# Optimization experiments

Measured on AMD Instinct MI355X. Metric: run time of the kernel, lower is better.

The kernel has to match this reference:

```python
import jax, jax.numpy as jnp
import numpy as np

EPS = 1e-5
SLOPE = 0.01  # LeakyReLU default
C = 512
C2 = C // 2
B, D, W, H = 2, 16, 16, 16


def _leaky(x):
    return jnp.where(x >= 0, x, SLOPE * x)


def _bn_c(x, g, b, rm, rv):
    # per-channel BN (eval mode) over axis 1 of a (B,C,...) tensor
    shape = (1, -1) + (1,) * (x.ndim - 2)
    inv = jax.lax.rsqrt(rv + EPS)
    return (x - rm.reshape(shape)) * (inv * g).reshape(shape) + b.reshape(shape)


def _bn_s(x, g, b, rm, rv):
    # scalar-feature BatchNorm1d(1) in eval mode
    return (x - rm[0]) * (jax.lax.rsqrt(rv[0] + EPS) * g[0]) + b[0]


def setup_inputs() -> dict:
    key = jax.random.key(0)
    ks = jax.random.split(key, 8)
    s = 0.02
    inp = {
        'x': jax.random.normal(ks[0], (B, C, D, W, H), jnp.float32),
        'topo_prompt': jax.random.normal(ks[1], (D, W, H, 6), jnp.float32) * s,
        # edge_aggregation_func: Linear(6,1)+BN1d(1)
        'w_ea': jax.random.normal(ks[2], (1, 6), jnp.float32) * s,
        'b_ea': jnp.zeros((1,), jnp.float32),
        'g_ea': jnp.ones((1,), jnp.float32), 'be_ea': jnp.zeros((1,), jnp.float32),
        'rm_ea': jnp.zeros((1,), jnp.float32), 'rv_ea': jnp.ones((1,), jnp.float32),
        # vertex_update_func: Linear(2C, C/2)+BN1d(C/2)
        'w_v': jax.random.normal(ks[3], (C2, 2 * C), jnp.float32) * s,
        'b_v': jnp.zeros((C2,), jnp.float32),
        'g_v': jnp.ones((C2,), jnp.float32), 'be_v': jnp.zeros((C2,), jnp.float32),
        'rm_v': jnp.zeros((C2,), jnp.float32), 'rv_v': jnp.ones((C2,), jnp.float32),
        # edge_update_func: Linear(2C, C/2)+BN1d(C/2)
        'w_e': jax.random.normal(ks[4], (C2, 2 * C), jnp.float32) * s,
        'b_e': jnp.zeros((C2,), jnp.float32),
        'g_e': jnp.ones((C2,), jnp.float32), 'be_e': jnp.zeros((C2,), jnp.float32),
        'rm_e': jnp.zeros((C2,), jnp.float32), 'rv_e': jnp.ones((C2,), jnp.float32),
        # update_edge_reduce_func: Linear(6,1)+BN1d(1)
        'w_r': jax.random.normal(ks[5], (1, 6), jnp.float32) * s,
        'b_r': jnp.zeros((1,), jnp.float32),
        'g_r': jnp.ones((1,), jnp.float32), 'be_r': jnp.zeros((1,), jnp.float32),
        'rm_r': jnp.zeros((1,), jnp.float32), 'rv_r': jnp.ones((1,), jnp.float32),
        # final_aggregation_layer: Conv3d(3C/2 -> C, k=1, bias=False)+BN3d(C)
        'w_f': jax.random.normal(ks[6], (C, C + C2), jnp.float32) * s,
        'g_f': jnp.ones((C,), jnp.float32), 'be_f': jnp.zeros((C,), jnp.float32),
        'rm_f': jnp.zeros((C,), jnp.float32), 'rv_f': jnp.ones((C,), jnp.float32),
    }
    return inp


def reference(x, topo_prompt,
              w_ea, b_ea, g_ea, be_ea, rm_ea, rv_ea,
              w_v, b_v, g_v, be_v, rm_v, rv_v,
              w_e, b_e, g_e, be_e, rm_e, rv_e,
              w_r, b_r, g_r, be_r, rm_r, rv_r,
              w_f, g_f, be_f, rm_f, rv_f):
    # 6-neighbor circular shifts: cat((x[-1:], x[:-1])) == roll(+1); cat((x[1:], x[:1])) == roll(-1)
    shifts = jnp.stack([
        jnp.roll(x, 1, axis=2), jnp.roll(x, -1, axis=2),
        jnp.roll(x, 1, axis=3), jnp.roll(x, -1, axis=3),
        jnp.roll(x, 1, axis=4), jnp.roll(x, -1, axis=4),
    ], axis=-1)  # (B,C,D,W,H,6)
    edge = shifts * x[..., None] + topo_prompt  # topo_prompt (D,W,H,6) broadcasts

    # edge aggregation: Linear(6->1) + BN1d(1) + LeakyReLU
    agg = jnp.einsum('bcdwhk,k->bcdwh', edge, w_ea[0]) + b_ea[0]
    agg = _leaky(_bn_s(agg, g_ea, be_ea, rm_ea, rv_ea))  # (B,C,D,W,H)

    # vertex update: Linear(2C->C/2) + BN + LeakyReLU
    feat_v = jnp.concatenate([x, agg], axis=1)  # (B,2C,D,W,H)
    uv = jnp.einsum('bcdwh,oc->bodwh', feat_v, w_v) + b_v[None, :, None, None, None]
    uv = _leaky(_bn_c(uv, g_v, be_v, rm_v, rv_v))  # (B,C/2,D,W,H)

    # edge update: cat(vertex x6, edge) on channel dim -> Linear(2C->C/2) + BN + LeakyReLU
    vrep = jnp.broadcast_to(x[..., None], x.shape + (6,))
    feat_e = jnp.concatenate([vrep, edge], axis=1)  # (B,2C,D,W,H,6)
    ue = jnp.einsum('bcdwhk,oc->bodwhk', feat_e, w_e) + b_e[None, :, None, None, None, None]
    ue = _leaky(_bn_c(ue, g_e, be_e, rm_e, rv_e))  # (B,C/2,D,W,H,6)

    # reduce 6 neighbors: Linear(6->1) + BN1d(1) + LeakyReLU
    ur = jnp.einsum('bodwhk,k->bodwh', ue, w_r[0]) + b_r[0]
    ur = _leaky(_bn_s(ur, g_r, be_r, rm_r, rv_r))  # (B,C/2,D,W,H)

    update_feature = uv * ur

    # final 1x1x1 conv (bias=False) + BN3d + LeakyReLU
    fused = jnp.concatenate([x, update_feature], axis=1)  # (B,3C/2,D,W,H)
    out = jnp.einsum('bcdwh,oc->bodwh', fused, w_f)
    out = _leaky(_bn_c(out, g_f, be_f, rm_f, rv_f))
    return out
```

## Files before the change

kernel.cpp:

```cpp
#include <hip/hip_runtime.h>

#define BATCH 2
#define C 512
#define C2 256
#define V 4096
#define NROWS 8192
#define EPS 1e-5f
#define SLOPE 0.01f

typedef __bf16 bf16;
typedef __bf16 bf16x8 __attribute__((ext_vector_type(8)));
typedef __bf16 bf16x4 __attribute__((ext_vector_type(4)));
typedef float  f32x4  __attribute__((ext_vector_type(4)));

__device__ __forceinline__ float leaky(float x) { return x >= 0.f ? x : SLOPE * x; }

__device__ __forceinline__ int nbr(int v, int k) {
    int h = v & 15, w = (v >> 4) & 15, d = v >> 8;
    switch (k) {
        case 0: return (v & 0x0FF) | (((d + 15) & 15) << 8);
        case 1: return (v & 0x0FF) | (((d + 1) & 15) << 8);
        case 2: return (v & 0xF0F) | (((w + 15) & 15) << 4);
        case 3: return (v & 0xF0F) | (((w + 1) & 15) << 4);
        case 4: return (v & 0xFF0) | ((h + 15) & 15);
        default: return (v & 0xFF0) | ((h + 1) & 15);
    }
}

__device__ __forceinline__ void gload16(const bf16* g, bf16* l) {
    __builtin_amdgcn_global_load_lds(
        (const __attribute__((address_space(1))) void*)g,
        (__attribute__((address_space(3))) void*)l, 16, 0, 0);
}

__device__ __forceinline__ void stage_gl64(bf16* buf, const bf16* srcbase, size_t ld,
                                           int kcol, int wv, int lane) {
    const int sslot = ((lane & 7) ^ (lane >> 3)) * 8;
    #pragma unroll
    for (int j = 0; j < 4; j++) {
        const int rl = wv * 32 + j * 8;
        gload16(srcbase + (size_t)(rl + (lane >> 3)) * ld + kcol + sslot,
                buf + rl * 64);
    }
}

__device__ __forceinline__ void mmstep64(const bf16* A, const bf16* B,
                                         f32x4 (&acc)[4][4], int abase, int bbase,
                                         int lr, int kg)
{
    #pragma unroll
    for (int sub = 0; sub < 2; sub++) {
        const int slot = ((sub * 4 + kg) ^ (lr & 7)) * 8;
        bf16x8 af[4], bv[4];
        #pragma unroll
        for (int mb = 0; mb < 4; mb++)
            af[mb] = *(const bf16x8*)(A + (abase + mb * 16 + lr) * 64 + slot);
        #pragma unroll
        for (int nb = 0; nb < 4; nb++)
            bv[nb] = *(const bf16x8*)(B + (bbase + nb * 16 + lr) * 64 + slot);
        #pragma unroll
        for (int mb = 0; mb < 4; mb++)
            #pragma unroll
            for (int nb = 0; nb < 4; nb++)
                acc[mb][nb] = __builtin_amdgcn_mfma_f32_16x16x32_bf16(af[mb], bv[nb], acc[mb][nb], 0, 0, 0);
    }
}

__global__ __launch_bounds__(256) void k_prep(
    const float* wv, const float* we, const float* wf,
    const float* w_ea, const float* b_ea, const float* g_ea, const float* be_ea,
    const float* rm_ea, const float* rv_ea,
    const float* b_v, const float* g_v, const float* be_v, const float* rm_v, const float* rv_v,
    const float* b_e, const float* g_e, const float* be_e, const float* rm_e, const float* rv_e,
    const float* w_r, const float* b_r, const float* g_r, const float* be_r,
    const float* rm_r, const float* rv_r,
    const float* g_f, const float* be_f, const float* rm_f, const float* rv_f,
    float* P, float* obv, float* obe, float* obf,
    bf16* wmain, bf16* we2, bf16* owf)
{
    int i = blockIdx.x * 256 + threadIdx.x;
    if (i < 524288) {
        int o = i >> 10, c = i & 1023;
        float val;
        if (o < 256) val = rsqrtf(rv_v[o] + EPS) * g_v[o] * wv[(size_t)o * 1024 + c];
        else {
            int oe = o - 256;
            val = (c < 512) ? rsqrtf(rv_e[oe] + EPS) * g_e[oe] * we[(size_t)oe * 1024 + c] : 0.f;
        }
        wmain[i] = (bf16)val;
    } else if (i < 655360) {
        int j = i - 524288; int o = j >> 9, c = j & 511;
        we2[j] = (bf16)(rsqrtf(rv_e[o] + EPS) * g_e[o] * we[(size_t)o * 1024 + 512 + c]);
    } else if (i < 1048576) {
        int j = i - 655360; int o = j / 768;
        owf[j] = (bf16)(rsqrtf(rv_f[o] + EPS) * g_f[o] * wf[j]);
    }
    if (blockIdx.x == 0) {
        int t = threadIdx.x;
        obf[t]       = be_f[t]       - rsqrtf(rv_f[t]       + EPS) * g_f[t]       * rm_f[t];
        obf[t + 256] = be_f[t + 256] - rsqrtf(rv_f[t + 256] + EPS) * g_f[t + 256] * rm_f[t + 256];
        float sv = rsqrtf(rv_v[t] + EPS) * g_v[t];
        obv[t] = sv * (b_v[t] - rm_v[t]) + be_v[t];
        float se = rsqrtf(rv_e[t] + EPS) * g_e[t];
        obe[t] = se * (b_e[t] - rm_e[t]) + be_e[t];
        if (t < 6) {
            float sa = rsqrtf(rv_ea[0] + EPS) * g_ea[0];
            P[t] = sa * w_ea[t];
            float sr = rsqrtf(rv_r[0] + EPS) * g_r[0];
            P[8 + t] = sr * w_r[t];
        }
        if (t == 6) {
            float sa = rsqrtf(rv_ea[0] + EPS) * g_ea[0];
            P[6] = sa * (b_ea[0] - rm_ea[0]) + be_ea[0];
            float sr = rsqrtf(rv_r[0] + EPS) * g_r[0];
            P[14] = sr * (b_r[0] - rm_r[0]) + be_r[0];
        }
    }
}

__global__ __launch_bounds__(256) void k_aggT(
    const float* __restrict__ x, const float* __restrict__ topo,
    const float* __restrict__ P,
    bf16* __restrict__ xT, bf16* __restrict__ aggT)
{
    __shared__ float T[64][65];
    const int t = threadIdx.x;
    const int b = blockIdx.z, ct = blockIdx.y * 64, vt = blockIdx.x * 64;
    const int cl = t >> 2;
    const int c  = ct + cl;
    const int vl0 = (t & 3) * 16;
    const int v0 = vt + vl0;
    const int w = (v0 >> 4) & 15, d = v0 >> 8;
    const float* xp = x + (((size_t)b * C + c) << 12);

    float xr[16], xd0[16], xd1[16], xw0[16], xw1[16];
    #pragma unroll
    for (int i = 0; i < 4; i++) {
        float4 a;
        a = ((const float4*)(xp + v0))[i];                        xr [4*i]=a.x; xr [4*i+1]=a.y; xr [4*i+2]=a.z; xr [4*i+3]=a.w;
        a = ((const float4*)(xp + (((d+15)&15)<<8) + (w<<4)))[i]; xd0[4*i]=a.x; xd0[4*i+1]=a.y; xd0[4*i+2]=a.z; xd0[4*i+3]=a.w;
        a = ((const float4*)(xp + (((d+ 1)&15)<<8) + (w<<4)))[i]; xd1[4*i]=a.x; xd1[4*i+1]=a.y; xd1[4*i+2]=a.z; xd1[4*i+3]=a.w;
        a = ((const float4*)(xp + (d<<8) + (((w+15)&15)<<4)))[i]; xw0[4*i]=a.x; xw0[4*i+1]=a.y; xw0[4*i+2]=a.z; xw0[4*i+3]=a.w;
        a = ((const float4*)(xp + (d<<8) + (((w+ 1)&15)<<4)))[i]; xw1[4*i]=a.x; xw1[4*i+1]=a.y; xw1[4*i+2]=a.z; xw1[4*i+3]=a.w;
    }

    #pragma unroll
    for (int p = 0; p < 2; ++p) {
        float val[16];
        if (p == 0) {
            #pragma unroll
            for (int j = 0; j < 16; j++) val[j] = xr[j];
        } else {
            #pragma unroll
            for (int j = 0; j < 16; j++) {
                const float* tp = topo + (size_t)(v0 + j) * 6;
                float s = P[6];
                s = fmaf(P[0], fmaf(xd0[j], xr[j], tp[0]), s);
                s = fmaf(P[1], fmaf(xd1[j], xr[j], tp[1]), s);
                s = fmaf(P[2], fmaf(xw0[j], xr[j], tp[2]), s);
                s = fmaf(P[3], fmaf(xw1[j], xr[j], tp[3]), s);
                s = fmaf(P[4], fmaf(xr[(j+15)&15], xr[j], tp[4]), s);
                s = fmaf(P[5], fmaf(xr[(j+ 1)&15], xr[j], tp[5]), s);
                val[j] = leaky(s);
            }
        }
        __syncthreads();
        #pragma unroll
        for (int j = 0; j < 16; j++) T[cl][vl0 + j] = val[j];
        __syncthreads();
        const int vr = t >> 2, c0 = (t & 3) * 16;
        bf16x8 lo, hi;
        #pragma unroll
        for (int i = 0; i < 8; i++) {
            lo[i] = (bf16)T[c0 + i][vr];
            hi[i] = (bf16)T[c0 + 8 + i][vr];
        }
        bf16* dst = (p == 0) ? xT : aggT;
        bf16* dp = dst + ((size_t)(b << 12) + vt + vr) * C + ct + c0;
        *(bf16x8*)dp = lo;
        *(bf16x8*)(dp + 8) = hi;
    }
}

template<bool MAIN>
__device__ __forceinline__ void gemm_body(
    int m0, int n0, int kk, int nsteps,
    const bf16* __restrict__ wA, size_t ldA,
    const bf16* __restrict__ xT, const bf16* __restrict__ aggT,
    const float* __restrict__ topo, const float* __restrict__ bvp,
    bf16* __restrict__ uvT, float* __restrict__ sxe, bf16* __restrict__ se,
    bf16 (*A)[128 * 64], bf16 (*B)[128 * 64])
{
    const int t = threadIdx.x, lane = t & 63;
    const int wv = t >> 6, wmi = wv >> 1, wni = wv & 1;
    const int lr = lane & 15, kg = lane >> 4;

    const bf16* wAb  = wA + (size_t)m0 * ldA;
    const bf16* xTb  = xT + (size_t)n0 * C;
    const bf16* agTb = aggT + (size_t)n0 * C;

    const int erow = t >> 1, ecol = (t & 1) * 32;
    const bf16* pBx = nullptr; const bf16* pB2 = nullptr; float tp = 0.f;
    int eslot[4];
    if (!MAIN) {
        const int rB = n0 + erow;
        const int vvv = rB & 4095, bb = rB >> 12;
        pBx = xT + (size_t)rB * C + ecol;
        pB2 = xT + (size_t)((bb << 12) | nbr(vvv, kk)) * C + ecol;
        tp = topo[vvv * 6 + kk];
        #pragma unroll
        for (int j = 0; j < 4; j++)
            eslot[j] = ((((t & 1) * 4 + j) ^ (erow & 7)) * 8);
    }

    f32x4 acc[4][4];
    #pragma unroll
    for (int mb = 0; mb < 4; mb++)
        #pragma unroll
        for (int nb = 0; nb < 4; nb++) acc[mb][nb] = 0.f;

    uint4 bx[4], bn[4];
    auto issueB = [&](int s) {
        #pragma unroll
        for (int j = 0; j < 4; j++) {
            bx[j] = *(const uint4*)(pBx + s * 64 + j * 8);
            bn[j] = *(const uint4*)(pB2 + s * 64 + j * 8);
        }
    };
    auto commitB = [&](int buf) {
        #pragma unroll
        for (int j = 0; j < 4; j++) {
            bf16x8 xa = *(bf16x8*)&bx[j], xn = *(bf16x8*)&bn[j];
            bf16x8 e;
            #pragma unroll
            for (int i = 0; i < 8; i++)
                e[i] = (bf16)fmaf((float)xa[i], (float)xn[i], tp);
            *(bf16x8*)(&B[buf][erow * 64 + eslot[j]]) = e;
        }
    };
    auto stageStep = [&](int buf, int s) {
        stage_gl64(A[buf], wAb, ldA, s * 64, wv, lane);
        if (MAIN) {
            const bf16* src = (s < 8) ? xTb : agTb;
            stage_gl64(B[buf], src, C, (s & 7) * 64, wv, lane);
        }
    };

    stageStep(0, 0);
    if (!MAIN) { issueB(0); commitB(0); if (nsteps > 1) issueB(1); }

    int cb = 0;
    #pragma unroll 1
    for (int s = 0; s < nsteps; ++s) {
        __syncthreads();
        if (s + 1 < nsteps) stageStep(cb ^ 1, s + 1);
        mmstep64(A[cb], B[cb], acc, wmi * 64, wni * 64, lr, kg);
        if (!MAIN && s + 1 < nsteps) {
            commitB(cb ^ 1);
            if (s + 2 < nsteps) issueB(s + 2);
        }
        cb ^= 1;
    }

    if (MAIN) {
        if (m0 < 256) {
            #pragma unroll
            for (int mb = 0; mb < 4; mb++) {
                const int o = m0 + wmi * 64 + mb * 16 + kg * 4;
                f32x4 bv4 = *(const f32x4*)(bvp + o);
                #pragma unroll
                for (int nb = 0; nb < 4; nb++) {
                    const int col = n0 + wni * 64 + nb * 16 + lr;
                    bf16x4 o4;
                    #pragma unroll
                    for (int q = 0; q < 4; q++)
                        o4[q] = (bf16)leaky(acc[mb][nb][q] + bv4[q]);
                    *(bf16x4*)(uvT + (size_t)col * C2 + o) = o4;
                }
            }
        } else {
            #pragma unroll
            for (int mb = 0; mb < 4; mb++) {
                const int o = (m0 - 256) + wmi * 64 + mb * 16 + kg * 4;
                #pragma unroll
                for (int nb = 0; nb < 4; nb++) {
                    const int col = n0 + wni * 64 + nb * 16 + lr;
                    *(f32x4*)(sxe + (size_t)col * C2 + o) = acc[mb][nb];
                }
            }
        }
    } else {
        #pragma unroll
        for (int mb = 0; mb < 4; mb++) {
            const int o = m0 + wmi * 64 + mb * 16 + kg * 4;
            #pragma unroll
            for (int nb = 0; nb < 4; nb++) {
                const int col = n0 + wni * 64 + nb * 16 + lr;
                bf16x4 o4;
                #pragma unroll
                for (int q = 0; q < 4; q++) o4[q] = (bf16)acc[mb][nb][q];
                *(bf16x4*)(se + ((size_t)kk * NROWS + col) * C2 + o) = o4;
            }
        }
    }
}

__global__ __launch_bounds__(256, 2) void k_gemm(
    const bf16* __restrict__ xT, const bf16* __restrict__ aggT,
    const bf16* __restrict__ wm, const bf16* __restrict__ we2,
    const float* __restrict__ bvp, const float* __restrict__ topo,
    bf16* __restrict__ uvT, float* __restrict__ sxe, bf16* __restrict__ se)
{
    __shared__ __align__(16) bf16 A[2][128 * 64];
    __shared__ __align__(16) bf16 B[2][128 * 64];
    const int lb = (blockIdx.x & 7) * 128 + (blockIdx.x >> 3);
    const int n0 = (lb >> 4) * 128;
    const int sub = lb & 15;
    if (sub < 4) {
        const int m0 = sub * 128;
        const int nsteps = (m0 < 256) ? 16 : 8;
        gemm_body<true>(m0, n0, 0, nsteps, wm, 1024, xT, aggT, topo, bvp,
                        uvT, sxe, nullptr, A, B);
    } else {
        const int e = sub - 4;
        const int kk = e >> 1, m0 = (e & 1) * 128;
        gemm_body<false>(m0, n0, kk, 8, we2, 512, xT, aggT, topo, bvp,
                         nullptr, nullptr, se, A, B);
    }
}

__global__ __launch_bounds__(256) void k_comb(
    const float* __restrict__ sxe, const bf16* __restrict__ se,
    const bf16* __restrict__ uvT, const float* __restrict__ bep,
    const float* __restrict__ P, bf16* __restrict__ updT)
{
    const int g = blockIdx.x * 256 + threadIdx.x;
    const int row = g >> 5, o0 = (g & 31) * 8;
    const size_t base = (size_t)row * C2 + o0;

    f32x4 sx0 = *(const f32x4*)(sxe + base);
    f32x4 sx1 = *(const f32x4*)(sxe + base + 4);
    f32x4 be0 = *(const f32x4*)(bep + o0);
    f32x4 be1 = *(const f32x4*)(bep + o0 + 4);
    float ur[8] = {};
    #pragma unroll
    for (int k = 0; k < 6; k++) {
        bf16x8 s8 = *(const bf16x8*)(se + (size_t)k * NROWS * C2 + base);
        const float wrk = P[8 + k];
        #pragma unroll
        for (int i = 0; i < 4; i++) {
            ur[i]     = fmaf(wrk, leaky(sx0[i] + (float)s8[i]     + be0[i]), ur[i]);
            ur[i + 4] = fmaf(wrk, leaky(sx1[i] + (float)s8[i + 4] + be1[i]), ur[i + 4]);
        }
    }
    const float brp = P[14];
    bf16x8 uv8 = *(const bf16x8*)(uvT + base);
    bf16x8 o8;
    #pragma unroll
    for (int i = 0; i < 8; i++)
        o8[i] = (bf16)((float)uv8[i] * leaky(ur[i] + brp));
    *(bf16x8*)(updT + base) = o8;
}

__global__ __launch_bounds__(256, 2) void k_out(
    const bf16* __restrict__ xT, const bf16* __restrict__ updT,
    const bf16* __restrict__ wf, const float* __restrict__ bfp,
    float* __restrict__ out)
{
    __shared__ __align__(16) bf16 A[2][128 * 64];
    __shared__ __align__(16) bf16 B[2][128 * 64];
    const int t = threadIdx.x, lane = t & 63;
    const int wv = t >> 6, wmi = wv >> 1, wni = wv & 1;
    const int lr = lane & 15, kg = lane >> 4;
    const int lb = (blockIdx.x & 7) * 32 + (blockIdx.x >> 3);
    const int n0 = (lb >> 2) * 128, m0 = (lb & 3) * 128;

    const bf16* wAb = wf   + (size_t)m0 * 768;
    const bf16* xTb = xT   + (size_t)n0 * C;
    const bf16* uTb = updT + (size_t)n0 * C2;

    f32x4 acc[4][4];
    #pragma unroll
    for (int mb = 0; mb < 4; mb++)
        #pragma unroll
        for (int nb = 0; nb < 4; nb++) acc[mb][nb] = 0.f;

    auto stageStep = [&](int buf, int s) {
        stage_gl64(A[buf], wAb, 768, s * 64, wv, lane);
        if (s < 8) stage_gl64(B[buf], xTb, C, s * 64, wv, lane);
        else       stage_gl64(B[buf], uTb, C2, (s - 8) * 64, wv, lane);
    };

    stageStep(0, 0);
    int cb = 0;
    #pragma unroll 1
    for (int s = 0; s < 12; ++s) {
        __syncthreads();
        if (s + 1 < 12) stageStep(cb ^ 1, s + 1);
        mmstep64(A[cb], B[cb], acc, wmi * 64, wni * 64, lr, kg);
        cb ^= 1;
    }

    #pragma unroll
    for (int mb = 0; mb < 4; mb++) {
        const int o = m0 + wmi * 64 + mb * 16 + kg * 4;
        f32x4 bf4 = *(const f32x4*)(bfp + o);
        #pragma unroll
        for (int nb = 0; nb < 4; nb++) {
            const int col = n0 + wni * 64 + nb * 16 + lr;
            const int b = col >> 12, v = col & 4095;
            #pragma unroll
            for (int q = 0; q < 4; q++)
                out[(((size_t)b * C + o + q) << 12) + v] = leaky(acc[mb][nb][q] + bf4[q]);
        }
    }
}

extern "C" void kernel_launch(void* const* d_in, const int* in_sizes, int n_in,
                              void* d_out, int out_size, void* d_ws, size_t ws_size,
                              hipStream_t stream)
{
    const float* x    = (const float*)d_in[0];
    const float* topo = (const float*)d_in[1];
    const float* w_ea = (const float*)d_in[2];
    const float* b_ea = (const float*)d_in[3];
    const float* g_ea = (const float*)d_in[4];
    const float* be_ea= (const float*)d_in[5];
    const float* rm_ea= (const float*)d_in[6];
    const float* rv_ea= (const float*)d_in[7];
    const float* w_v  = (const float*)d_in[8];
    const float* b_v  = (const float*)d_in[9];
    const float* g_v  = (const float*)d_in[10];
    const float* be_v = (const float*)d_in[11];
    const float* rm_v = (const float*)d_in[12];
    const float* rv_v = (const float*)d_in[13];
    const float* w_e  = (const float*)d_in[14];
    const float* b_e  = (const float*)d_in[15];
    const float* g_e  = (const float*)d_in[16];
    const float* be_e = (const float*)d_in[17];
    const float* rm_e = (const float*)d_in[18];
    const float* rv_e = (const float*)d_in[19];
    const float* w_r  = (const float*)d_in[20];
    const float* b_r  = (const float*)d_in[21];
    const float* g_r  = (const float*)d_in[22];
    const float* be_r = (const float*)d_in[23];
    const float* rm_r = (const float*)d_in[24];
    const float* rv_r = (const float*)d_in[25];
    const float* w_f  = (const float*)d_in[26];
    const float* g_f  = (const float*)d_in[27];
    const float* be_f = (const float*)d_in[28];
    const float* rm_f = (const float*)d_in[29];
    const float* rv_f = (const float*)d_in[30];

    char* base = (char*)d_ws;
    size_t off = 0;
    auto take = [&](size_t bytes) { size_t r = off; off = (off + bytes + 255) & ~(size_t)255; return r; };
    float* P    = (float*)(base + take(64 * 4));
    float* bvp  = (float*)(base + take(256 * 4));
    float* bep  = (float*)(base + take(256 * 4));
    float* bfp  = (float*)(base + take(512 * 4));
    bf16*  wmp  = (bf16*)(base + take((size_t)524288 * 2));
    bf16*  we2p = (bf16*)(base + take((size_t)131072 * 2));
    bf16*  wfp  = (bf16*)(base + take((size_t)393216 * 2));
    bf16*  xT   = (bf16*)(base + take((size_t)NROWS * C * 2));
    bf16*  aggT = (bf16*)(base + take((size_t)NROWS * C * 2));
    bf16*  uvT  = (bf16*)(base + take((size_t)NROWS * C2 * 2));
    bf16*  updT = (bf16*)(base + take((size_t)NROWS * C2 * 2));
    float* sxe  = (float*)(base + take((size_t)NROWS * C2 * 4));
    bf16*  se   = (bf16*)(base + take((size_t)6 * NROWS * C2 * 2));

    k_prep<<<4096, 256, 0, stream>>>(
        w_v, w_e, w_f,
        w_ea, b_ea, g_ea, be_ea, rm_ea, rv_ea,
        b_v, g_v, be_v, rm_v, rv_v,
        b_e, g_e, be_e, rm_e, rv_e,
        w_r, b_r, g_r, be_r, rm_r, rv_r,
        g_f, be_f, rm_f, rv_f,
        P, bvp, bep, bfp, wmp, we2p, wfp);

    k_aggT<<<dim3(64, 8, 2), 256, 0, stream>>>(x, topo, P, xT, aggT);

    k_gemm<<<dim3(1024), 256, 0, stream>>>(xT, aggT, wmp, we2p, bvp, topo, uvT, sxe, se);
    k_comb<<<dim3(NROWS * C2 / 8 / 256), 256, 0, stream>>>(sxe, se, uvT, bep, P, updT);
    k_out<<<dim3(256), 256, 0, stream>>>(xT, updT, wfp, bfp, (float*)d_out);
}
```

Measured before the change: 96.05 us.

## Enlarge gemm tiles to 256x128 with 512 threads and explicit waitcnt pipelining

The fused gemm kernel moves from 128x128 tiles with 256 threads to 256x128 tiles with 512 threads. Each block now covers the full output channel range per job type, which halves the block count and lets one B tile be reused across twice as many A rows. The single __syncthreads per step is replaced by manual s_waitcnt vmcnt/lgkmcnt plus two s_barriers so the next stage's loads stay in flight during the MFMA step; the output kernel gets the same barrier scheme. This raises LDS use and register pressure per block and depends on hand-counted outstanding loads being correct.

```diff
diff --git a/kernel.cpp b/kernel.cpp
--- a/kernel.cpp
+++ b/kernel.cpp
@@ -33,6 +33,24 @@
         (__attribute__((address_space(3))) void*)l, 16, 0, 0);
 }
 
+__device__ __forceinline__ void stageA256(bf16* buf, const bf16* src, size_t ld,
+                                          int kcol, int wv, int lane) {
+    const int sslot = ((lane & 7) ^ (lane >> 3)) * 8;
+    #pragma unroll
+    for (int j = 0; j < 4; j++) {
+        const int rl = wv * 32 + j * 8;
+        gload16(src + (size_t)(rl + (lane >> 3)) * ld + kcol + sslot, buf + rl * 64);
+    }
+}
+__device__ __forceinline__ void stageB128(bf16* buf, const bf16* src, size_t ld,
+                                          int kcol, int wv, int lane) {
+    const int sslot = ((lane & 7) ^ (lane >> 3)) * 8;
+    #pragma unroll
+    for (int j = 0; j < 2; j++) {
+        const int rl = wv * 16 + j * 8;
+        gload16(src + (size_t)(rl + (lane >> 3)) * ld + kcol + sslot, buf + rl * 64);
+    }
+}
 __device__ __forceinline__ void stage_gl64(bf16* buf, const bf16* srcbase, size_t ld,
                                            int kcol, int wv, int lane) {
     const int sslot = ((lane & 7) ^ (lane >> 3)) * 8;
@@ -189,28 +207,29 @@
     const bf16* __restrict__ xT, const bf16* __restrict__ aggT,
     const float* __restrict__ topo, const float* __restrict__ bvp,
     bf16* __restrict__ uvT, float* __restrict__ sxe, bf16* __restrict__ se,
-    bf16 (*A)[128 * 64], bf16 (*B)[128 * 64])
-{
-    const int t = threadIdx.x, lane = t & 63;
-    const int wv = t >> 6, wmi = wv >> 1, wni = wv & 1;
+    bf16 (*A)[256 * 64], bf16 (*B)[128 * 64])
+{
+    const int t = threadIdx.x, lane = t & 63, wv = t >> 6;
+    const int wmi = wv >> 1, wni = wv & 1;
     const int lr = lane & 15, kg = lane >> 4;
 
     const bf16* wAb  = wA + (size_t)m0 * ldA;
     const bf16* xTb  = xT + (size_t)n0 * C;
     const bf16* agTb = aggT + (size_t)n0 * C;
 
-    const int erow = t >> 1, ecol = (t & 1) * 32;
+    const int erow = t >> 2;
     const bf16* pBx = nullptr; const bf16* pB2 = nullptr; float tp = 0.f;
-    int eslot[4];
+    int es0 = 0, es1 = 0;
     if (!MAIN) {
         const int rB = n0 + erow;
         const int vvv = rB & 4095, bb = rB >> 12;
+        const int ecol = (t & 3) * 16;
         pBx = xT + (size_t)rB * C + ecol;
         pB2 = xT + (size_t)((bb << 12) | nbr(vvv, kk)) * C + ecol;
         tp = topo[vvv * 6 + kk];
-        #pragma unroll
-        for (int j = 0; j < 4; j++)
-            eslot[j] = ((((t & 1) * 4 + j) ^ (erow & 7)) * 8);
+        const int g0 = (t & 3) * 2;
+        es0 = ((g0 ^ (erow & 7)) * 8);
+        es1 = (((g0 + 1) ^ (erow & 7)) * 8);
     }
 
     f32x4 acc[4][4];
@@ -219,54 +238,60 @@
         #pragma unroll
         for (int nb = 0; nb < 4; nb++) acc[mb][nb] = 0.f;
 
-    uint4 bx[4], bn[4];
+    uint4 bx0, bx1, bn0, bn1;
     auto issueB = [&](int s) {
-        #pragma unroll
-        for (int j = 0; j < 4; j++) {
-            bx[j] = *(const uint4*)(pBx + s * 64 + j * 8);
-            bn[j] = *(const uint4*)(pB2 + s * 64 + j * 8);
-        }
+        bx0 = *(const uint4*)(pBx + s * 64);
+        bx1 = *(const uint4*)(pBx + s * 64 + 8);
+        bn0 = *(const uint4*)(pB2 + s * 64);
+        bn1 = *(const uint4*)(pB2 + s * 64 + 8);
     };
-    auto commitB = [&](int buf) {
-        #pragma unroll
-        for (int j = 0; j < 4; j++) {
-            bf16x8 xa = *(bf16x8*)&bx[j], xn = *(bf16x8*)&bn[j];
-            bf16x8 e;
-            #pragma unroll
-            for (int i = 0; i < 8; i++)
-                e[i] = (bf16)fmaf((float)xa[i], (float)xn[i], tp);
-            *(bf16x8*)(&B[buf][erow * 64 + eslot[j]]) = e;
-        }
+    auto commitB = [&](bf16* Bb) {
+        bf16x8 xa = *(bf16x8*)&bx0, xn = *(bf16x8*)&bn0, e;
+        #pragma unroll
+        for (int i = 0; i < 8; i++) e[i] = (bf16)fmaf((float)xa[i], (float)xn[i], tp);
+        *(bf16x8*)(&Bb[erow * 64 + es0]) = e;
+        xa = *(bf16x8*)&bx1; xn = *(bf16x8*)&bn1;
+        #pragma unroll
+        for (int i = 0; i < 8; i++) e[i] = (bf16)fmaf((float)xa[i], (float)xn[i], tp);
+        *(bf16x8*)(&Bb[erow * 64 + es1]) = e;
     };
     auto stageStep = [&](int buf, int s) {
-        stage_gl64(A[buf], wAb, ldA, s * 64, wv, lane);
+        stageA256(A[buf], wAb, ldA, s * 64, wv, lane);
         if (MAIN) {
             const bf16* src = (s < 8) ? xTb : agTb;
-            stage_gl64(B[buf], src, C, (s & 7) * 64, wv, lane);
+            stageB128(B[buf], src, C, (s & 7) * 64, wv, lane);
         }
     };
 
+    if (!MAIN) issueB(0);
     stageStep(0, 0);
-    if (!MAIN) { issueB(0); commitB(0); if (nsteps > 1) issueB(1); }
-
-    int cb = 0;
+    if (!MAIN) { commitB(B[0]); if (nsteps > 1) issueB(1); }
+
     #pragma unroll 1
     for (int s = 0; s < nsteps; ++s) {
-        __syncthreads();
-        if (s + 1 < nsteps) stageStep(cb ^ 1, s + 1);
-        mmstep64(A[cb], B[cb], acc, wmi * 64, wni * 64, lr, kg);
-        if (!MAIN && s + 1 < nsteps) {
-            commitB(cb ^ 1);
+        const bool more = (s + 1 < nsteps);
+        if (more) stageStep((s + 1) & 1, s + 1);
+        if (!MAIN) asm volatile("s_waitcnt lgkmcnt(0)" ::: "memory");
+        if (more) {
+            if (MAIN) asm volatile("s_waitcnt vmcnt(6)" ::: "memory");
+            else      asm volatile("s_waitcnt vmcnt(8)" ::: "memory");
+        } else {
+            asm volatile("s_waitcnt vmcnt(0)" ::: "memory");
+        }
+        __builtin_amdgcn_s_barrier();
+        mmstep64(A[s & 1], B[s & 1], acc, wmi * 64, wni * 64, lr, kg);
+        if (!MAIN && more) {
+            commitB(B[(s + 1) & 1]);
             if (s + 2 < nsteps) issueB(s + 2);
         }
-        cb ^= 1;
+        __builtin_amdgcn_s_barrier();
     }
 
     if (MAIN) {
-        if (m0 < 256) {
+        if (m0 == 0) {
             #pragma unroll
             for (int mb = 0; mb < 4; mb++) {
-                const int o = m0 + wmi * 64 + mb * 16 + kg * 4;
+                const int o = wmi * 64 + mb * 16 + kg * 4;
                 f32x4 bv4 = *(const f32x4*)(bvp + o);
                 #pragma unroll
                 for (int nb = 0; nb < 4; nb++) {
@@ -281,7 +306,7 @@
         } else {
             #pragma unroll
             for (int mb = 0; mb < 4; mb++) {
-                const int o = (m0 - 256) + wmi * 64 + mb * 16 + kg * 4;
+                const int o = wmi * 64 + mb * 16 + kg * 4;
                 #pragma unroll
                 for (int nb = 0; nb < 4; nb++) {
                     const int col = n0 + wni * 64 + nb * 16 + lr;
@@ -292,7 +317,7 @@
     } else {
         #pragma unroll
         for (int mb = 0; mb < 4; mb++) {
-            const int o = m0 + wmi * 64 + mb * 16 + kg * 4;
+            const int o = wmi * 64 + mb * 16 + kg * 4;
             #pragma unroll
             for (int nb = 0; nb < 4; nb++) {
                 const int col = n0 + wni * 64 + nb * 16 + lr;
@@ -305,26 +330,24 @@
     }
 }
 
-__global__ __launch_bounds__(256, 2) void k_gemm(
+__global__ __launch_bounds__(512, 2) void k_gemm(
     const bf16* __restrict__ xT, const bf16* __restrict__ aggT,
     const bf16* __restrict__ wm, const bf16* __restrict__ we2,
     const float* __restrict__ bvp, const float* __restrict__ topo,
     bf16* __restrict__ uvT, float* __restrict__ sxe, bf16* __restrict__ se)
 {
-    __shared__ __align__(16) bf16 A[2][128 * 64];
+    __shared__ __align__(16) bf16 A[2][256 * 64];
     __shared__ __align__(16) bf16 B[2][128 * 64];
-    const int lb = (blockIdx.x & 7) * 128 + (blockIdx.x >> 3);
-    const int n0 = (lb >> 4) * 128;
-    const int sub = lb & 15;
-    if (sub < 4) {
-        const int m0 = sub * 128;
-        const int nsteps = (m0 < 256) ? 16 : 8;
+    const int lb = (blockIdx.x & 7) * 64 + (blockIdx.x >> 3);
+    const int n0 = (lb >> 3) * 128;
+    const int sub = lb & 7;
+    if (sub < 2) {
+        const int m0 = sub * 256;
+        const int nsteps = (sub == 0) ? 16 : 8;
         gemm_body<true>(m0, n0, 0, nsteps, wm, 1024, xT, aggT, topo, bvp,
                         uvT, sxe, nullptr, A, B);
     } else {
-        const int e = sub - 4;
-        const int kk = e >> 1, m0 = (e & 1) * 128;
-        gemm_body<false>(m0, n0, kk, 8, we2, 512, xT, aggT, topo, bvp,
+        gemm_body<false>(0, n0, sub - 2, 8, we2, 512, xT, aggT, topo, bvp,
                          nullptr, nullptr, se, A, B);
     }
 }
@@ -392,13 +415,15 @@
     };
 
     stageStep(0, 0);
-    int cb = 0;
     #pragma unroll 1
     for (int s = 0; s < 12; ++s) {
-        __syncthreads();
-        if (s + 1 < 12) stageStep(cb ^ 1, s + 1);
-        mmstep64(A[cb], B[cb], acc, wmi * 64, wni * 64, lr, kg);
-        cb ^= 1;
+        const bool more = (s + 1 < 12);
+        if (more) stageStep((s + 1) & 1, s + 1);
+        if (more) asm volatile("s_waitcnt vmcnt(8)" ::: "memory");
+        else      asm volatile("s_waitcnt vmcnt(0)" ::: "memory");
+        __builtin_amdgcn_s_barrier();
+        mmstep64(A[s & 1], B[s & 1], acc, wmi * 64, wni * 64, lr, kg);
+        __builtin_amdgcn_s_barrier();
     }
 
     #pragma unroll
@@ -480,7 +505,7 @@
 
     k_aggT<<<dim3(64, 8, 2), 256, 0, stream>>>(x, topo, P, xT, aggT);
 
-    k_gemm<<<dim3(1024), 256, 0, stream>>>(xT, aggT, wmp, we2p, bvp, topo, uvT, sxe, se);
+    k_gemm<<<dim3(512), 512, 0, stream>>>(xT, aggT, wmp, we2p, bvp, topo, uvT, sxe, se);
     k_comb<<<dim3(NROWS * C2 / 8 / 256), 256, 0, stream>>>(sxe, se, uvT, bep, P, updT);
     k_out<<<dim3(256), 256, 0, stream>>>(xT, updT, wfp, bfp, (float*)d_out);
 }
```

Measured after the change: 100.1 us. 4.2% more time.

## Enlarge GEMM tiles to 256x256 with 8 waves and phased prefetch pipeline

Applied to the files above, without the earlier changes.

The fused GEMM kernel now uses 256x256 output tiles computed by 512-thread blocks (8 waves, each owning a 128x64 sub-tile), instead of 128x128 tiles with 4 waves. Each K step is split into four phases that interleave LDS fragment loads, staggered global prefetch of the next stage, and MFMA bursts under raised wave priority, with explicit barriers and waitcnts. The aim is more operand reuse per LDS byte and better overlap of memory and compute. In exchange the grid shrinks from 1024 to 256 blocks, LDS use doubles to 128 KB per block, and accumulator register pressure doubles, which may limit occupancy and leave some CUs underused on the 256-CU part.

```diff
diff --git a/kernel.cpp b/kernel.cpp
--- a/kernel.cpp
+++ b/kernel.cpp
@@ -33,6 +33,15 @@
         (__attribute__((address_space(3))) void*)l, 16, 0, 0);
 }
 
+__device__ __forceinline__ void stage_half(bf16* buf, const bf16* src, size_t ld,
+                                           int kcol, int wv, int lane, int jbase) {
+    const int sslot = ((lane & 7) ^ (lane >> 3)) * 8;
+    #pragma unroll
+    for (int j = 0; j < 2; j++) {
+        const int rl = wv * 32 + (jbase + j) * 8;
+        gload16(src + (size_t)(rl + (lane >> 3)) * ld + kcol + sslot, buf + rl * 64);
+    }
+}
 __device__ __forceinline__ void stage_gl64(bf16* buf, const bf16* srcbase, size_t ld,
                                            int kcol, int wv, int lane) {
     const int sslot = ((lane & 7) ^ (lane >> 3)) * 8;
@@ -182,151 +191,172 @@
     }
 }
 
-template<bool MAIN>
-__device__ __forceinline__ void gemm_body(
-    int m0, int n0, int kk, int nsteps,
-    const bf16* __restrict__ wA, size_t ldA,
+template<int TYPE>
+__device__ __forceinline__ void gemm8p(
+    int n0, int kk, int nsteps,
+    const bf16* __restrict__ wAb, size_t ldA,
     const bf16* __restrict__ xT, const bf16* __restrict__ aggT,
     const float* __restrict__ topo, const float* __restrict__ bvp,
     bf16* __restrict__ uvT, float* __restrict__ sxe, bf16* __restrict__ se,
-    bf16 (*A)[128 * 64], bf16 (*B)[128 * 64])
-{
-    const int t = threadIdx.x, lane = t & 63;
-    const int wv = t >> 6, wmi = wv >> 1, wni = wv & 1;
+    bf16* Alds, bf16* Blds)
+{
+    const int t = threadIdx.x, lane = t & 63, wv = t >> 6;
+    const int wmi = wv >> 2, wni = wv & 3;
     const int lr = lane & 15, kg = lane >> 4;
 
-    const bf16* wAb  = wA + (size_t)m0 * ldA;
     const bf16* xTb  = xT + (size_t)n0 * C;
     const bf16* agTb = aggT + (size_t)n0 * C;
 
-    const int erow = t >> 1, ecol = (t & 1) * 32;
+    const int er = t >> 1, ech = t & 1;
     const bf16* pBx = nullptr; const bf16* pB2 = nullptr; float tp = 0.f;
-    int eslot[4];
-    if (!MAIN) {
-        const int rB = n0 + erow;
+    if (TYPE == 2) {
+        const int rB = n0 + er;
         const int vvv = rB & 4095, bb = rB >> 12;
-        pBx = xT + (size_t)rB * C + ecol;
-        pB2 = xT + (size_t)((bb << 12) | nbr(vvv, kk)) * C + ecol;
+        pBx = xT + (size_t)rB * C + ech * 32;
+        pB2 = xT + (size_t)((bb << 12) | nbr(vvv, kk)) * C + ech * 32;
         tp = topo[vvv * 6 + kk];
-        #pragma unroll
-        for (int j = 0; j < 4; j++)
-            eslot[j] = ((((t & 1) * 4 + j) ^ (erow & 7)) * 8);
-    }
-
-    f32x4 acc[4][4];
-    #pragma unroll
-    for (int mb = 0; mb < 4; mb++)
-        #pragma unroll
-        for (int nb = 0; nb < 4; nb++) acc[mb][nb] = 0.f;
-
-    uint4 bx[4], bn[4];
-    auto issueB = [&](int s) {
+    }
+
+    f32x4 acc[8][4];
+    #pragma unroll
+    for (int mf = 0; mf < 8; mf++)
+        #pragma unroll
+        for (int nf = 0; nf < 4; nf++) acc[mf][nf] = 0.f;
+
+    uint4 exa[4], exn[4];
+    auto issueE = [&](int s) {
         #pragma unroll
         for (int j = 0; j < 4; j++) {
-            bx[j] = *(const uint4*)(pBx + s * 64 + j * 8);
-            bn[j] = *(const uint4*)(pB2 + s * 64 + j * 8);
+            exa[j] = *(const uint4*)(pBx + s * 64 + j * 8);
+            exn[j] = *(const uint4*)(pB2 + s * 64 + j * 8);
         }
     };
-    auto commitB = [&](int buf) {
+    auto commitE = [&](bf16* Bb) {
         #pragma unroll
         for (int j = 0; j < 4; j++) {
-            bf16x8 xa = *(bf16x8*)&bx[j], xn = *(bf16x8*)&bn[j];
-            bf16x8 e;
+            bf16x8 xa = *(bf16x8*)&exa[j], xn = *(bf16x8*)&exn[j], e;
             #pragma unroll
             for (int i = 0; i < 8; i++)
                 e[i] = (bf16)fmaf((float)xa[i], (float)xn[i], tp);
-            *(bf16x8*)(&B[buf][erow * 64 + eslot[j]]) = e;
+            *(bf16x8*)(&Bb[er * 64 + (((ech * 4 + j) ^ (er & 7)) * 8)]) = e;
         }
     };
-    auto stageStep = [&](int buf, int s) {
-        stage_gl64(A[buf], wAb, ldA, s * 64, wv, lane);
-        if (MAIN) {
-            const bf16* src = (s < 8) ? xTb : agTb;
-            stage_gl64(B[buf], src, C, (s & 7) * 64, wv, lane);
-        }
+    auto stageB = [&](bf16* Bb, int s) {
+        const bf16* src; int bc;
+        if (TYPE == 0) { src = (s < 8) ? xTb : agTb; bc = (s & 7) * 64; }
+        else           { src = xTb; bc = s * 64; }
+        stage_half(Bb, src, C, bc, wv, lane, 0);
+        stage_half(Bb, src, C, bc, wv, lane, 2);
     };
 
-    stageStep(0, 0);
-    if (!MAIN) { issueB(0); commitB(0); if (nsteps > 1) issueB(1); }
-
-    int cb = 0;
+    stage_half(Alds, wAb, ldA, 0, wv, lane, 0);
+    stage_half(Alds, wAb, ldA, 0, wv, lane, 2);
+    if (TYPE == 2) {
+        issueE(0);
+        asm volatile("s_waitcnt vmcnt(0)" ::: "memory");
+        commitE(Blds);
+        asm volatile("s_waitcnt lgkmcnt(0)" ::: "memory");
+    } else {
+        stageB(Blds, 0);
+        asm volatile("s_waitcnt vmcnt(0)" ::: "memory");
+    }
+    __builtin_amdgcn_s_barrier();
+
     #pragma unroll 1
     for (int s = 0; s < nsteps; ++s) {
-        __syncthreads();
-        if (s + 1 < nsteps) stageStep(cb ^ 1, s + 1);
-        mmstep64(A[cb], B[cb], acc, wmi * 64, wni * 64, lr, kg);
-        if (!MAIN && s + 1 < nsteps) {
-            commitB(cb ^ 1);
-            if (s + 2 < nsteps) issueB(s + 2);
-        }
-        cb ^= 1;
-    }
-
-    if (MAIN) {
-        if (m0 < 256) {
-            #pragma unroll
-            for (int mb = 0; mb < 4; mb++) {
-                const int o = m0 + wmi * 64 + mb * 16 + kg * 4;
-                f32x4 bv4 = *(const f32x4*)(bvp + o);
+        const bool more = (s + 1 < nsteps);
+        const bf16* Ab = Alds + (s & 1) * (256 * 64);
+        const bf16* Bb = Blds + (s & 1) * (256 * 64);
+        bf16* An = Alds + ((s + 1) & 1) * (256 * 64);
+        bf16* Bn = Blds + ((s + 1) & 1) * (256 * 64);
+        #pragma unroll
+        for (int p = 0; p < 4; ++p) {
+            const int h = p & 1, np = p >> 1;
+            bf16x8 af[2][4], bvv[2][2];
+            #pragma unroll
+            for (int sub = 0; sub < 2; sub++) {
+                const int slot = ((sub * 4 + kg) ^ (lr & 7)) * 8;
                 #pragma unroll
-                for (int nb = 0; nb < 4; nb++) {
-                    const int col = n0 + wni * 64 + nb * 16 + lr;
-                    bf16x4 o4;
-                    #pragma unroll
-                    for (int q = 0; q < 4; q++)
-                        o4[q] = (bf16)leaky(acc[mb][nb][q] + bv4[q]);
-                    *(bf16x4*)(uvT + (size_t)col * C2 + o) = o4;
+                for (int mi = 0; mi < 4; mi++)
+                    af[sub][mi] = *(const bf16x8*)(Ab + (wmi * 128 + (h * 4 + mi) * 16 + lr) * 64 + slot);
+                #pragma unroll
+                for (int ni = 0; ni < 2; ni++)
+                    bvv[sub][ni] = *(const bf16x8*)(Bb + (wni * 64 + (np * 2 + ni) * 16 + lr) * 64 + slot);
+            }
+            if (more) {
+                if (p < 2) stage_half(An, wAb, ldA, (s + 1) * 64, wv, lane, p * 2);
+                else if (p == 2) {
+                    if (TYPE == 2) issueE(s + 1);
+                    else           stageB(Bn, s + 1);
                 }
             }
-        } else {
-            #pragma unroll
-            for (int mb = 0; mb < 4; mb++) {
-                const int o = (m0 - 256) + wmi * 64 + mb * 16 + kg * 4;
+            __builtin_amdgcn_s_barrier();
+            asm volatile("s_waitcnt lgkmcnt(0)" ::: "memory");
+            __builtin_amdgcn_s_setprio(1);
+            #pragma unroll
+            for (int sub = 0; sub < 2; sub++)
                 #pragma unroll
-                for (int nb = 0; nb < 4; nb++) {
-                    const int col = n0 + wni * 64 + nb * 16 + lr;
-                    *(f32x4*)(sxe + (size_t)col * C2 + o) = acc[mb][nb];
+                for (int mi = 0; mi < 4; mi++)
+                    #pragma unroll
+                    for (int ni = 0; ni < 2; ni++)
+                        acc[h * 4 + mi][np * 2 + ni] =
+                            __builtin_amdgcn_mfma_f32_16x16x32_bf16(
+                                af[sub][mi], bvv[sub][ni], acc[h * 4 + mi][np * 2 + ni], 0, 0, 0);
+            __builtin_amdgcn_s_setprio(0);
+            if (p == 3 && more) {
+                asm volatile("s_waitcnt vmcnt(0)" ::: "memory");
+                if (TYPE == 2) {
+                    commitE(Bn);
+                    asm volatile("s_waitcnt lgkmcnt(0)" ::: "memory");
                 }
             }
-        }
-    } else {
-        #pragma unroll
-        for (int mb = 0; mb < 4; mb++) {
-            const int o = m0 + wmi * 64 + mb * 16 + kg * 4;
-            #pragma unroll
-            for (int nb = 0; nb < 4; nb++) {
-                const int col = n0 + wni * 64 + nb * 16 + lr;
+            __builtin_amdgcn_s_barrier();
+        }
+    }
+
+    #pragma unroll
+    for (int mf = 0; mf < 8; mf++) {
+        const int o = wmi * 128 + mf * 16 + kg * 4;
+        f32x4 bv4;
+        if (TYPE == 0) bv4 = *(const f32x4*)(bvp + o);
+        #pragma unroll
+        for (int nf = 0; nf < 4; nf++) {
+            const int col = n0 + wni * 64 + nf * 16 + lr;
+            if (TYPE == 0) {
                 bf16x4 o4;
                 #pragma unroll
-                for (int q = 0; q < 4; q++) o4[q] = (bf16)acc[mb][nb][q];
+                for (int q = 0; q < 4; q++)
+                    o4[q] = (bf16)leaky(acc[mf][nf][q] + bv4[q]);
+                *(bf16x4*)(uvT + (size_t)col * C2 + o) = o4;
+            } else if (TYPE == 1) {
+                *(f32x4*)(sxe + (size_t)col * C2 + o) = acc[mf][nf];
+            } else {
+                bf16x4 o4;
+                #pragma unroll
+                for (int q = 0; q < 4; q++) o4[q] = (bf16)acc[mf][nf][q];
                 *(bf16x4*)(se + ((size_t)kk * NROWS + col) * C2 + o) = o4;
             }
         }
     }
 }
 
-__global__ __launch_bounds__(256, 2) void k_gemm(
+__global__ __launch_bounds__(512, 2) void k_gemm(
     const bf16* __restrict__ xT, const bf16* __restrict__ aggT,
     const bf16* __restrict__ wm, const bf16* __restrict__ we2,
     const float* __restrict__ bvp, const float* __restrict__ topo,
     bf16* __restrict__ uvT, float* __restrict__ sxe, bf16* __restrict__ se)
 {
-    __shared__ __align__(16) bf16 A[2][128 * 64];
-    __shared__ __align__(16) bf16 B[2][128 * 64];
-    const int lb = (blockIdx.x & 7) * 128 + (blockIdx.x >> 3);
-    const int n0 = (lb >> 4) * 128;
-    const int sub = lb & 15;
-    if (sub < 4) {
-        const int m0 = sub * 128;
-        const int nsteps = (m0 < 256) ? 16 : 8;
-        gemm_body<true>(m0, n0, 0, nsteps, wm, 1024, xT, aggT, topo, bvp,
-                        uvT, sxe, nullptr, A, B);
-    } else {
-        const int e = sub - 4;
-        const int kk = e >> 1, m0 = (e & 1) * 128;
-        gemm_body<false>(m0, n0, kk, 8, we2, 512, xT, aggT, topo, bvp,
-                         nullptr, nullptr, se, A, B);
-    }
+    __shared__ __align__(16) bf16 Alds[2 * 256 * 64];
+    __shared__ __align__(16) bf16 Blds[2 * 256 * 64];
+    const int lb = (blockIdx.x & 7) * 32 + (blockIdx.x >> 3);
+    const int panel = lb >> 3, sub = lb & 7;
+    const int n0 = panel * 256;
+    if (sub == 0)
+        gemm8p<0>(n0, 0, 16, wm, 1024, xT, aggT, topo, bvp, uvT, sxe, se, Alds, Blds);
+    else if (sub == 1)
+        gemm8p<1>(n0, 0, 8, wm + (size_t)256 * 1024, 1024, xT, aggT, topo, bvp, uvT, sxe, se, Alds, Blds);
+    else
+        gemm8p<2>(n0, sub - 2, 8, we2, 512, xT, aggT, topo, bvp, uvT, sxe, se, Alds, Blds);
 }
 
 __global__ __launch_bounds__(256) void k_comb(
@@ -480,7 +510,7 @@
 
     k_aggT<<<dim3(64, 8, 2), 256, 0, stream>>>(x, topo, P, xT, aggT);
 
-    k_gemm<<<dim3(1024), 256, 0, stream>>>(xT, aggT, wmp, we2p, bvp, topo, uvT, sxe, se);
+    k_gemm<<<dim3(256), 512, 0, stream>>>(xT, aggT, wmp, we2p, bvp, topo, uvT, sxe, se);
     k_comb<<<dim3(NROWS * C2 / 8 / 256), 256, 0, stream>>>(sxe, se, uvT, bep, P, updT);
     k_out<<<dim3(256), 256, 0, stream>>>(xT, updT, wfp, bfp, (float*)d_out);
 }
```

Measured after the change: 97.31 us. No clear change (+1.3%).

## Fuse vertex/edge GEMMs and neighbor reduction into one register-resident kernel

Applied to the files above, without the earlier changes.

Replaces the tiled GEMM kernel and the separate combine kernel with one fused kernel. Each 512-thread block owns 32 rows and walks all K-steps in turn: the vertex GEMM, the shared x-part of the edge GEMM, and the six per-neighbor edge GEMMs. It applies bias, LeakyReLU and the 6-to-1 reduction in registers after each phase. This removes the global writes and reads of the large per-neighbor edge buffer, the fp32 shared-term buffer and the uv buffer, and one kernel launch. In exchange, every block re-streams the full weight matrices with a narrow 32-row N tile, uses about 144KB of LDS per block at one block per CU, and runs with low occupancy.

```diff
diff --git a/kernel.cpp b/kernel.cpp
--- a/kernel.cpp
+++ b/kernel.cpp
@@ -182,184 +182,132 @@
     }
 }
 
-template<bool MAIN>
-__device__ __forceinline__ void gemm_body(
-    int m0, int n0, int kk, int nsteps,
-    const bf16* __restrict__ wA, size_t ldA,
+__global__ __launch_bounds__(512, 1) void k_fused(
     const bf16* __restrict__ xT, const bf16* __restrict__ aggT,
-    const float* __restrict__ topo, const float* __restrict__ bvp,
-    bf16* __restrict__ uvT, float* __restrict__ sxe, bf16* __restrict__ se,
-    bf16 (*A)[128 * 64], bf16 (*B)[128 * 64])
-{
-    const int t = threadIdx.x, lane = t & 63;
-    const int wv = t >> 6, wmi = wv >> 1, wni = wv & 1;
+    const bf16* __restrict__ wm, const bf16* __restrict__ we2,
+    const float* __restrict__ bvp, const float* __restrict__ bep,
+    const float* __restrict__ P, const float* __restrict__ topo,
+    bf16* __restrict__ updT)
+{
+    __shared__ __align__(16) bf16 Ab[2][256 * 128];
+    __shared__ __align__(16) bf16 Bb[2][32 * 128];
+    const int t = threadIdx.x, lane = t & 63, wv = t >> 6;
+    const int wmi = wv >> 1, wni = wv & 1;
     const int lr = lane & 15, kg = lane >> 4;
-
-    const bf16* wAb  = wA + (size_t)m0 * ldA;
+    const int n0 = blockIdx.x * 32;
+
     const bf16* xTb  = xT + (size_t)n0 * C;
     const bf16* agTb = aggT + (size_t)n0 * C;
 
-    const int erow = t >> 1, ecol = (t & 1) * 32;
-    const bf16* pBx = nullptr; const bf16* pB2 = nullptr; float tp = 0.f;
-    int eslot[4];
-    if (!MAIN) {
-        const int rB = n0 + erow;
-        const int vvv = rB & 4095, bb = rB >> 12;
-        pBx = xT + (size_t)rB * C + ecol;
-        pB2 = xT + (size_t)((bb << 12) | nbr(vvv, kk)) * C + ecol;
-        tp = topo[vvv * 6 + kk];
-        #pragma unroll
-        for (int j = 0; j < 4; j++)
-            eslot[j] = ((((t & 1) * 4 + j) ^ (erow & 7)) * 8);
-    }
-
-    f32x4 acc[4][4];
-    #pragma unroll
-    for (int mb = 0; mb < 4; mb++)
-        #pragma unroll
-        for (int nb = 0; nb < 4; nb++) acc[mb][nb] = 0.f;
-
-    uint4 bx[4], bn[4];
-    auto issueB = [&](int s) {
-        #pragma unroll
-        for (int j = 0; j < 4; j++) {
-            bx[j] = *(const uint4*)(pBx + s * 64 + j * 8);
-            bn[j] = *(const uint4*)(pB2 + s * 64 + j * 8);
+    const int er = t >> 4, eslot = t & 15;
+    const int colB = n0 + er, vvv = colB & 4095, bb = colB >> 12;
+
+    f32x4 bvv[4], bee[4];
+    #pragma unroll
+    for (int mf = 0; mf < 4; mf++) {
+        const int o = wmi * 64 + mf * 16 + kg * 4;
+        bvv[mf] = *(const f32x4*)(bvp + o);
+        bee[mf] = *(const f32x4*)(bep + o);
+    }
+
+    f32x4 acc[4], uvr[4], sxe[4], ur[4];
+    #pragma unroll
+    for (int mf = 0; mf < 4; mf++) { acc[mf] = 0.f; uvr[mf] = 0.f; sxe[mf] = 0.f; ur[mf] = 0.f; }
+
+    uint4 exa, exn; float tpc = 0.f;
+    auto stageStep = [&](int buf, int st) {
+        const bf16* wA; size_t ldA; int kcA;
+        if (st < 8)       { wA = wm;                     ldA = 1024; kcA = st * 128; }
+        else if (st < 12) { wA = wm + (size_t)262144;    ldA = 1024; kcA = (st - 8) * 128; }
+        else              { wA = we2;                    ldA = 512;  kcA = ((st - 12) & 3) * 128; }
+        #pragma unroll
+        for (int j = 0; j < 8; j++) {
+            const int rowbase = wv * 32 + j * 4;
+            const int row = rowbase + (lane >> 4);
+            const int ss = ((lane & 15) ^ (row & 7)) * 8;
+            gload16(wA + (size_t)row * ldA + kcA + ss, &Ab[buf][rowbase * 128]);
+        }
+        if (st < 12) {
+            const bf16* bs; int kc;
+            if (st < 4)      { bs = xTb;  kc = st * 128; }
+            else if (st < 8) { bs = agTb; kc = (st - 4) * 128; }
+            else             { bs = xTb;  kc = (st - 8) * 128; }
+            const int rowbase = wv * 4;
+            const int row = rowbase + (lane >> 4);
+            const int ss = ((lane & 15) ^ (row & 7)) * 8;
+            gload16(bs + (size_t)row * C + kc + ss, &Bb[buf][rowbase * 128]);
+        } else {
+            const int k = (st - 12) >> 2, kc = ((st - 12) & 3) * 128;
+            const int rn = (bb << 12) | nbr(vvv, k);
+            tpc = topo[vvv * 6 + k];
+            exa = *(const uint4*)(xT + (size_t)colB * C + kc + eslot * 8);
+            exn = *(const uint4*)(xT + (size_t)rn * C + kc + eslot * 8);
         }
     };
-    auto commitB = [&](int buf) {
-        #pragma unroll
-        for (int j = 0; j < 4; j++) {
-            bf16x8 xa = *(bf16x8*)&bx[j], xn = *(bf16x8*)&bn[j];
-            bf16x8 e;
-            #pragma unroll
-            for (int i = 0; i < 8; i++)
-                e[i] = (bf16)fmaf((float)xa[i], (float)xn[i], tp);
-            *(bf16x8*)(&B[buf][erow * 64 + eslot[j]]) = e;
-        }
+    auto commitE = [&](int buf) {
+        bf16x8 xa = *(bf16x8*)&exa, xn = *(bf16x8*)&exn, e;
+        #pragma unroll
+        for (int i = 0; i < 8; i++)
+            e[i] = (bf16)fmaf((float)xa[i], (float)xn[i], tpc);
+        *(bf16x8*)(&Bb[buf][er * 128 + ((eslot ^ (er & 7)) * 8)]) = e;
     };
-    auto stageStep = [&](int buf, int s) {
-        stage_gl64(A[buf], wAb, ldA, s * 64, wv, lane);
-        if (MAIN) {
-            const bf16* src = (s < 8) ? xTb : agTb;
-            stage_gl64(B[buf], src, C, (s & 7) * 64, wv, lane);
+    auto mm = [&](int buf) {
+        #pragma unroll
+        for (int sub = 0; sub < 4; sub++) {
+            const int slot = ((sub * 4 + kg) ^ (lr & 7)) * 8;
+            bf16x8 bv = *(const bf16x8*)(&Bb[buf][(wni * 16 + lr) * 128 + slot]);
+            #pragma unroll
+            for (int mf = 0; mf < 4; mf++) {
+                bf16x8 af = *(const bf16x8*)(&Ab[buf][(wmi * 64 + mf * 16 + lr) * 128 + slot]);
+                acc[mf] = __builtin_amdgcn_mfma_f32_16x16x32_bf16(af, bv, acc[mf], 0, 0, 0);
+            }
         }
     };
 
     stageStep(0, 0);
-    if (!MAIN) { issueB(0); commitB(0); if (nsteps > 1) issueB(1); }
-
     int cb = 0;
     #pragma unroll 1
-    for (int s = 0; s < nsteps; ++s) {
+    for (int st = 0; st < 36; ++st) {
         __syncthreads();
-        if (s + 1 < nsteps) stageStep(cb ^ 1, s + 1);
-        mmstep64(A[cb], B[cb], acc, wmi * 64, wni * 64, lr, kg);
-        if (!MAIN && s + 1 < nsteps) {
-            commitB(cb ^ 1);
-            if (s + 2 < nsteps) issueB(s + 2);
+        if (st + 1 < 36) stageStep(cb ^ 1, st + 1);
+        mm(cb);
+        if (st + 1 < 36 && st + 1 >= 12) commitE(cb ^ 1);
+        if (st == 7) {
+            #pragma unroll
+            for (int mf = 0; mf < 4; mf++) {
+                #pragma unroll
+                for (int q = 0; q < 4; q++)
+                    uvr[mf][q] = leaky(acc[mf][q] + bvv[mf][q]);
+                acc[mf] = 0.f;
+            }
+        } else if (st == 11) {
+            #pragma unroll
+            for (int mf = 0; mf < 4; mf++) { sxe[mf] = acc[mf]; acc[mf] = 0.f; }
+        } else if (st >= 15 && ((st - 15) & 3) == 0) {
+            const int k = (st - 12) >> 2;
+            const float wrk = P[8 + k];
+            #pragma unroll
+            for (int mf = 0; mf < 4; mf++) {
+                #pragma unroll
+                for (int q = 0; q < 4; q++)
+                    ur[mf][q] = fmaf(wrk, leaky(sxe[mf][q] + acc[mf][q] + bee[mf][q]), ur[mf][q]);
+                acc[mf] = 0.f;
+            }
         }
         cb ^= 1;
     }
 
-    if (MAIN) {
-        if (m0 < 256) {
-            #pragma unroll
-            for (int mb = 0; mb < 4; mb++) {
-                const int o = m0 + wmi * 64 + mb * 16 + kg * 4;
-                f32x4 bv4 = *(const f32x4*)(bvp + o);
-                #pragma unroll
-                for (int nb = 0; nb < 4; nb++) {
-                    const int col = n0 + wni * 64 + nb * 16 + lr;
-                    bf16x4 o4;
-                    #pragma unroll
-                    for (int q = 0; q < 4; q++)
-                        o4[q] = (bf16)leaky(acc[mb][nb][q] + bv4[q]);
-                    *(bf16x4*)(uvT + (size_t)col * C2 + o) = o4;
-                }
-            }
-        } else {
-            #pragma unroll
-            for (int mb = 0; mb < 4; mb++) {
-                const int o = (m0 - 256) + wmi * 64 + mb * 16 + kg * 4;
-                #pragma unroll
-                for (int nb = 0; nb < 4; nb++) {
-                    const int col = n0 + wni * 64 + nb * 16 + lr;
-                    *(f32x4*)(sxe + (size_t)col * C2 + o) = acc[mb][nb];
-                }
-            }
-        }
-    } else {
-        #pragma unroll
-        for (int mb = 0; mb < 4; mb++) {
-            const int o = m0 + wmi * 64 + mb * 16 + kg * 4;
-            #pragma unroll
-            for (int nb = 0; nb < 4; nb++) {
-                const int col = n0 + wni * 64 + nb * 16 + lr;
-                bf16x4 o4;
-                #pragma unroll
-                for (int q = 0; q < 4; q++) o4[q] = (bf16)acc[mb][nb][q];
-                *(bf16x4*)(se + ((size_t)kk * NROWS + col) * C2 + o) = o4;
-            }
-        }
-    }
-}
-
-__global__ __launch_bounds__(256, 2) void k_gemm(
-    const bf16* __restrict__ xT, const bf16* __restrict__ aggT,
-    const bf16* __restrict__ wm, const bf16* __restrict__ we2,
-    const float* __restrict__ bvp, const float* __restrict__ topo,
-    bf16* __restrict__ uvT, float* __restrict__ sxe, bf16* __restrict__ se)
-{
-    __shared__ __align__(16) bf16 A[2][128 * 64];
-    __shared__ __align__(16) bf16 B[2][128 * 64];
-    const int lb = (blockIdx.x & 7) * 128 + (blockIdx.x >> 3);
-    const int n0 = (lb >> 4) * 128;
-    const int sub = lb & 15;
-    if (sub < 4) {
-        const int m0 = sub * 128;
-        const int nsteps = (m0 < 256) ? 16 : 8;
-        gemm_body<true>(m0, n0, 0, nsteps, wm, 1024, xT, aggT, topo, bvp,
-                        uvT, sxe, nullptr, A, B);
-    } else {
-        const int e = sub - 4;
-        const int kk = e >> 1, m0 = (e & 1) * 128;
-        gemm_body<false>(m0, n0, kk, 8, we2, 512, xT, aggT, topo, bvp,
-                         nullptr, nullptr, se, A, B);
-    }
-}
-
-__global__ __launch_bounds__(256) void k_comb(
-    const float* __restrict__ sxe, const bf16* __restrict__ se,
-    const bf16* __restrict__ uvT, const float* __restrict__ bep,
-    const float* __restrict__ P, bf16* __restrict__ updT)
-{
-    const int g = blockIdx.x * 256 + threadIdx.x;
-    const int row = g >> 5, o0 = (g & 31) * 8;
-    const size_t base = (size_t)row * C2 + o0;
-
-    f32x4 sx0 = *(const f32x4*)(sxe + base);
-    f32x4 sx1 = *(const f32x4*)(sxe + base + 4);
-    f32x4 be0 = *(const f32x4*)(bep + o0);
-    f32x4 be1 = *(const f32x4*)(bep + o0 + 4);
-    float ur[8] = {};
-    #pragma unroll
-    for (int k = 0; k < 6; k++) {
-        bf16x8 s8 = *(const bf16x8*)(se + (size_t)k * NROWS * C2 + base);
-        const float wrk = P[8 + k];
-        #pragma unroll
-        for (int i = 0; i < 4; i++) {
-            ur[i]     = fmaf(wrk, leaky(sx0[i] + (float)s8[i]     + be0[i]), ur[i]);
-            ur[i + 4] = fmaf(wrk, leaky(sx1[i] + (float)s8[i + 4] + be1[i]), ur[i + 4]);
-        }
-    }
     const float brp = P[14];
-    bf16x8 uv8 = *(const bf16x8*)(uvT + base);
-    bf16x8 o8;
-    #pragma unroll
-    for (int i = 0; i < 8; i++)
-        o8[i] = (bf16)((float)uv8[i] * leaky(ur[i] + brp));
-    *(bf16x8*)(updT + base) = o8;
+    #pragma unroll
+    for (int mf = 0; mf < 4; mf++) {
+        const int o = wmi * 64 + mf * 16 + kg * 4;
+        const int col = n0 + wni * 16 + lr;
+        bf16x4 o4;
+        #pragma unroll
+        for (int q = 0; q < 4; q++)
+            o4[q] = (bf16)(uvr[mf][q] * leaky(ur[mf][q] + brp));
+        *(bf16x4*)(updT + (size_t)col * C2 + o) = o4;
+    }
 }
 
 __global__ __launch_bounds__(256, 2) void k_out(
@@ -464,10 +412,7 @@
     bf16*  wfp  = (bf16*)(base + take((size_t)393216 * 2));
     bf16*  xT   = (bf16*)(base + take((size_t)NROWS * C * 2));
     bf16*  aggT = (bf16*)(base + take((size_t)NROWS * C * 2));
-    bf16*  uvT  = (bf16*)(base + take((size_t)NROWS * C2 * 2));
     bf16*  updT = (bf16*)(base + take((size_t)NROWS * C2 * 2));
-    float* sxe  = (float*)(base + take((size_t)NROWS * C2 * 4));
-    bf16*  se   = (bf16*)(base + take((size_t)6 * NROWS * C2 * 2));
 
     k_prep<<<4096, 256, 0, stream>>>(
         w_v, w_e, w_f,
@@ -480,7 +425,7 @@
 
     k_aggT<<<dim3(64, 8, 2), 256, 0, stream>>>(x, topo, P, xT, aggT);
 
-    k_gemm<<<dim3(1024), 256, 0, stream>>>(xT, aggT, wmp, we2p, bvp, topo, uvT, sxe, se);
-    k_comb<<<dim3(NROWS * C2 / 8 / 256), 256, 0, stream>>>(sxe, se, uvT, bep, P, updT);
+    k_fused<<<dim3(256), 512, 0, stream>>>(xT, aggT, wmp, we2p, bvp, bep, P, topo, updT);
+
     k_out<<<dim3(256), 256, 0, stream>>>(xT, updT, wfp, bfp, (float*)d_out);
 }
```

Measured after the change: 117.7 us. 1.22x slower.
